# Kernel optimization log

Hardware: AMD Instinct MI355X
Metric: run time of the kernel (lower is better)

The kernel has to match this reference:

```python
import math
import jax, jax.numpy as jnp
import numpy as np

H, DK = 16, 64            # n_heads, d_kv
NUM_BUCKETS, MAX_DIST = 32, 128


def _relative_position_buckets(S):
    # Bidirectional (encoder) T5 bucketization of relative positions.
    ctx = jnp.arange(S, dtype=jnp.int32)[:, None]      # query positions
    mem = jnp.arange(S, dtype=jnp.int32)[None, :]      # key positions
    rp = mem - ctx                                     # [S, S]
    nb = NUM_BUCKETS // 2
    rb = (rp > 0).astype(jnp.int32) * nb
    n = jnp.abs(rp)
    max_exact = nb // 2
    is_small = n < max_exact
    large = max_exact + (
        jnp.log(jnp.maximum(n, 1).astype(jnp.float32) / max_exact)
        / math.log(MAX_DIST / max_exact)
        * (nb - max_exact)
    ).astype(jnp.int32)
    large = jnp.minimum(large, nb - 1)
    return rb + jnp.where(is_small, n, large)          # [S, S] int32


def setup_inputs() -> dict:
    key = jax.random.key(0)
    ks = jax.random.split(key, 6)
    B, S, D = 4, 1024, 1024
    inner = H * DK
    std = 0.02
    return {
        "hidden_states": jax.random.normal(ks[0], (B, S, D), jnp.float32),
        "Wq": jax.random.normal(ks[1], (inner, D), jnp.float32) * std,
        "Wk": jax.random.normal(ks[2], (inner, D), jnp.float32) * std,
        "Wv": jax.random.normal(ks[3], (inner, D), jnp.float32) * std,
        "Wo": jax.random.normal(ks[4], (D, inner), jnp.float32) * std,
        "rel_bias": jax.random.normal(ks[5], (NUM_BUCKETS, H), jnp.float32) * std,
    }


def reference(hidden_states, Wq, Wk, Wv, Wo, rel_bias):
    B, S, D = hidden_states.shape

    def proj(W):  # bias-free linear + split heads -> [B, H, S, DK]
        return (hidden_states @ W.T).reshape(B, S, H, DK).transpose(0, 2, 1, 3)

    q, k, v = proj(Wq), proj(Wk), proj(Wv)
    # T5: NO 1/sqrt(d) scaling
    scores = jnp.einsum("bhqd,bhkd->bhqk", q, k)       # [B, H, S, S]
    bias = rel_bias[_relative_position_buckets(S)]     # [S, S, H]
    scores = scores + bias.transpose(2, 0, 1)[None]    # broadcast over batch
    attn = jax.nn.softmax(scores, axis=-1)
    ctx = jnp.einsum("bhqk,bhkd->bhqd", attn, v)       # [B, H, S, DK]
    ctx = ctx.transpose(0, 2, 1, 3).reshape(B, S, H * DK)
    return ctx @ Wo.T                                  # [B, S, D]
```

## Files before the change

kernel.cpp:

```cpp
#include <hip/hip_runtime.h>

typedef _Float16 half8 __attribute__((ext_vector_type(8)));
typedef _Float16 half4_t __attribute__((ext_vector_type(4)));
typedef float f32x4 __attribute__((ext_vector_type(4)));

#define GK 1024
#define MEG (1024 * 1024)
#define LOG2E 1.44269504088896f

#define GLD16(gptr, lptr) \
    __builtin_amdgcn_global_load_lds((const __attribute__((address_space(1))) void*)(gptr), \
                                     (__attribute__((address_space(3))) void*)(lptr), 16, 0, 0)

__global__ void cvt_all_kernel(const float* __restrict__ hidden,
                               const float* __restrict__ Wq,
                               const float* __restrict__ Wk,
                               const float* __restrict__ Wv,
                               const float* __restrict__ Wo,
                               _Float16* __restrict__ ws) {
    int b = blockIdx.x;
    const float* src;
    _Float16* dst;
    if (b < 4096)      { src = hidden; dst = ws; }
    else if (b < 5120) { src = Wq; dst = ws + 4 * MEG; b -= 4096; }
    else if (b < 6144) { src = Wk; dst = ws + 5 * MEG; b -= 5120; }
    else if (b < 7168) { src = Wv; dst = ws + 6 * MEG; b -= 6144; }
    else               { src = Wo; dst = ws + 7 * MEG; b -= 7168; }
    int i = (b * 256 + threadIdx.x) * 4;
    f32x4 v = *(const f32x4*)(src + i);
    half4_t h;
    h[0] = (_Float16)v[0]; h[1] = (_Float16)v[1];
    h[2] = (_Float16)v[2]; h[3] = (_Float16)v[3];
    *(half4_t*)(dst + i) = h;
}

__global__ __launch_bounds__(256) void gemm_qkv_kernel(
    const _Float16* __restrict__ A,
    const _Float16* __restrict__ B0,
    const _Float16* __restrict__ B1,
    const _Float16* __restrict__ B2,
    _Float16* __restrict__ O0,
    _Float16* __restrict__ O1,
    _Float16* __restrict__ O2)
{
    int z = blockIdx.z;
    const _Float16* Bw = (z == 0) ? B0 : ((z == 1) ? B1 : B2);
    _Float16* Oh = (z == 0) ? O0 : ((z == 1) ? O1 : O2);

    __shared__ __attribute__((aligned(16))) _Float16 sA[2][128][32];
    __shared__ __attribute__((aligned(16))) _Float16 sB[2][128][32];

    const int tid = threadIdx.x;
    const int wave = tid >> 6, lane = tid & 63;
    const int quad = lane >> 4, l16 = lane & 15;
    const int wr = wave >> 1, wc = wave & 1;
    const int M0 = blockIdx.y * 128, N0 = blockIdx.x * 128;

    const int rl = lane >> 2;
    const int cl = (lane & 3) * 8;
    const size_t aRow0 = (size_t)(M0 + wave * 16 + rl) * GK + cl;
    const size_t aRow1 = aRow0 + (size_t)64 * GK;
    const size_t bRow0 = (size_t)(N0 + wave * 16 + rl) * GK + cl;
    const size_t bRow1 = bRow0 + (size_t)64 * GK;
    _Float16* ldsA[2][2] = {{&sA[0][wave * 16][0], &sA[0][64 + wave * 16][0]},
                            {&sA[1][wave * 16][0], &sA[1][64 + wave * 16][0]}};
    _Float16* ldsB[2][2] = {{&sB[0][wave * 16][0], &sB[0][64 + wave * 16][0]},
                            {&sB[1][wave * 16][0], &sB[1][64 + wave * 16][0]}};

    f32x4 acc[4][4] = {};

    for (int kt = 0; kt < GK / 64; ++kt) {
        const int ko = kt * 64;
        #pragma unroll
        for (int c = 0; c < 2; ++c) {
            GLD16(A + aRow0 + ko + c * 32, ldsA[c][0]);
            GLD16(A + aRow1 + ko + c * 32, ldsA[c][1]);
            GLD16(Bw + bRow0 + ko + c * 32, ldsB[c][0]);
            GLD16(Bw + bRow1 + ko + c * 32, ldsB[c][1]);
        }
        __syncthreads();
        #pragma unroll
        for (int c = 0; c < 2; ++c) {
            half8 af[4], bf[4];
            #pragma unroll
            for (int i = 0; i < 4; ++i)
                af[i] = *(const half8*)&sA[c][wr * 64 + i * 16 + l16][quad * 8];
            #pragma unroll
            for (int j = 0; j < 4; ++j)
                bf[j] = *(const half8*)&sB[c][wc * 64 + j * 16 + l16][quad * 8];
            #pragma unroll
            for (int i = 0; i < 4; ++i)
                #pragma unroll
                for (int j = 0; j < 4; ++j)
                    acc[i][j] = __builtin_amdgcn_mfma_f32_16x16x32_f16(af[i], bf[j], acc[i][j], 0, 0, 0);
        }
        __syncthreads();
    }

    #pragma unroll
    for (int i = 0; i < 4; ++i) {
        #pragma unroll
        for (int j = 0; j < 4; ++j) {
            #pragma unroll
            for (int r = 0; r < 4; ++r) {
                int m = M0 + wr * 64 + i * 16 + quad * 4 + r;
                int n = N0 + wc * 64 + j * 16 + l16;
                int b = m >> 10, s = m & 1023, hh = n >> 6, d = n & 63;
                Oh[((size_t)((b * 16 + hh) * 1024 + s)) * 64 + d] = (_Float16)acc[i][j][r];
            }
        }
    }
}

__global__ __launch_bounds__(256) void gemm_o_kernel(
    const _Float16* __restrict__ A,
    const _Float16* __restrict__ Bw,
    float* __restrict__ Of)
{
    __shared__ __attribute__((aligned(16))) _Float16 sA[2][64][32];
    __shared__ __attribute__((aligned(16))) _Float16 sB[2][128][32];

    const int tid = threadIdx.x;
    const int wave = tid >> 6, lane = tid & 63;
    const int quad = lane >> 4, l16 = lane & 15;
    const int M0 = blockIdx.y * 64, N0 = blockIdx.x * 128;

    const int rl = lane >> 2;
    const int cl = (lane & 3) * 8;
    const size_t aRow  = (size_t)(M0 + wave * 16 + rl) * GK + cl;
    const size_t bRow0 = (size_t)(N0 + wave * 16 + rl) * GK + cl;
    const size_t bRow1 = bRow0 + (size_t)64 * GK;
    _Float16* ldsA[2]    = {&sA[0][wave * 16][0], &sA[1][wave * 16][0]};
    _Float16* ldsB[2][2] = {{&sB[0][wave * 16][0], &sB[0][64 + wave * 16][0]},
                            {&sB[1][wave * 16][0], &sB[1][64 + wave * 16][0]}};

    f32x4 acc[4][2] = {};

    for (int kt = 0; kt < GK / 64; ++kt) {
        const int ko = kt * 64;
        #pragma unroll
        for (int c = 0; c < 2; ++c) {
            GLD16(A + aRow + ko + c * 32, ldsA[c]);
            GLD16(Bw + bRow0 + ko + c * 32, ldsB[c][0]);
            GLD16(Bw + bRow1 + ko + c * 32, ldsB[c][1]);
        }
        __syncthreads();
        #pragma unroll
        for (int c = 0; c < 2; ++c) {
            half8 af[4], bf[2];
            #pragma unroll
            for (int i = 0; i < 4; ++i)
                af[i] = *(const half8*)&sA[c][i * 16 + l16][quad * 8];
            #pragma unroll
            for (int j = 0; j < 2; ++j)
                bf[j] = *(const half8*)&sB[c][wave * 32 + j * 16 + l16][quad * 8];
            #pragma unroll
            for (int i = 0; i < 4; ++i)
                #pragma unroll
                for (int j = 0; j < 2; ++j)
                    acc[i][j] = __builtin_amdgcn_mfma_f32_16x16x32_f16(af[i], bf[j], acc[i][j], 0, 0, 0);
        }
        __syncthreads();
    }

    #pragma unroll
    for (int i = 0; i < 4; ++i) {
        #pragma unroll
        for (int j = 0; j < 2; ++j) {
            #pragma unroll
            for (int r = 0; r < 4; ++r) {
                int m = M0 + i * 16 + quad * 4 + r;
                int n = N0 + wave * 32 + j * 16 + l16;
                Of[(size_t)m * 1024 + n] = acc[i][j][r];
            }
        }
    }
}

__global__ __launch_bounds__(256) void transpose_v_kernel(
    const _Float16* __restrict__ V, _Float16* __restrict__ VT) {
    __shared__ __attribute__((aligned(16))) _Float16 sT[64][72];
    const int s0 = blockIdx.x * 64;
    const int bh = blockIdx.y;
    const _Float16* Vb = V + (size_t)bh * 1024 * 64 + (size_t)s0 * 64;
    _Float16* Tb = VT + (size_t)bh * 64 * 1024 + s0;
    const int r = threadIdx.x >> 3;
    const int c8 = (threadIdx.x & 7) * 8;
    #pragma unroll
    for (int p = 0; p < 2; ++p) {
        const int row = p * 32 + r;
        half8 v = *(const half8*)(Vb + (size_t)row * 64 + c8);
        #pragma unroll
        for (int e = 0; e < 8; ++e) sT[c8 + e][row] = v[e];
    }
    __syncthreads();
    #pragma unroll
    for (int p = 0; p < 2; ++p) {
        const int d = p * 32 + r;
        half8 o = *(const half8*)&sT[d][c8];
        *(half8*)(Tb + (size_t)d * 1024 + c8) = o;
    }
}

__global__ __launch_bounds__(256) void attn_kernel(
    const _Float16* __restrict__ Q,
    const _Float16* __restrict__ K,
    const _Float16* __restrict__ VT,
    const float* __restrict__ rel_bias,
    _Float16* __restrict__ ctx)
{
    const int S = 1024;
    const int qt = blockIdx.x;
    const int q0 = qt * 64;
    const int h = blockIdx.y;
    const int b = blockIdx.z;
    const int bh = b * 16 + h;
    const _Float16* Qh = Q + (size_t)bh * S * 64;
    const _Float16* Kh = K + (size_t)bh * S * 64;
    const _Float16* VTh = VT + (size_t)bh * 64 * S;

    __shared__ __attribute__((aligned(16))) _Float16 sQ[64][72];
    __shared__ __attribute__((aligned(16))) _Float16 sK[64][72];
    __shared__ __attribute__((aligned(16))) _Float16 sVt[64][72];
    __shared__ __attribute__((aligned(16))) _Float16 sP[4][16][72];
    __shared__ _Float16 sBias[1088];

    const int tid = threadIdx.x;
    const int wave = tid >> 6, lane = tid & 63;
    const int quad = lane >> 4, l16 = lane & 15;

    {
        int r = tid >> 3, c = (tid & 7) * 8;
        *(half8*)&sQ[r][c]      = *(const half8*)(Qh + (size_t)(q0 + r) * 64 + c);
        *(half8*)&sQ[r + 32][c] = *(const half8*)(Qh + (size_t)(q0 + r + 32) * 64 + c);
    }
    for (int i = tid; i < 1087; i += 256) {
        int delta = i - (q0 + 63);
        int rb = (delta > 0) ? 16 : 0;
        int n = (delta < 0) ? -delta : delta;
        int bucket;
        if (n < 8) bucket = rb + n;
        else bucket = rb + 8 + (n >= 12) + (n >= 16) + (n >= 23) + (n >= 32)
                             + (n >= 46) + (n >= 64) + (n >= 91);
        sBias[i] = (_Float16)rel_bias[bucket * 16 + h];
    }
    __syncthreads();

    half8 qf0 = *(const half8*)&sQ[wave * 16 + l16][quad * 8];
    half8 qf1 = *(const half8*)&sQ[wave * 16 + l16][32 + quad * 8];

    const int sr = tid >> 3;
    const int sc_ = (tid & 7) * 8;
    const _Float16* kp0 = Kh + (size_t)sr * 64 + sc_;
    const _Float16* kp1 = kp0 + (size_t)32 * 64;
    const _Float16* vp0 = VTh + (size_t)sr * S + sc_;
    const _Float16* vp1 = vp0 + (size_t)32 * S;
    _Float16* sKw0 = &sK[sr][sc_];
    _Float16* sKw1 = &sK[sr + 32][sc_];
    _Float16* sVw0 = &sVt[sr][sc_];
    _Float16* sVw1 = &sVt[sr + 32][sc_];

    half8 rk0 = *(const half8*)kp0;
    half8 rk1 = *(const half8*)kp1;
    half8 rv0 = *(const half8*)vp0;
    half8 rv1 = *(const half8*)vp1;
    kp0 += 4096; kp1 += 4096; vp0 += 64; vp1 += 64;

    float m_run = -INFINITY, l_run = 0.0f;
    f32x4 acc[4] = {};

    for (int kt = 0; kt < 16; ++kt) {
        __syncthreads();
        *(half8*)sKw0 = rk0;
        *(half8*)sKw1 = rk1;
        *(half8*)sVw0 = rv0;
        *(half8*)sVw1 = rv1;
        __syncthreads();
        if (kt < 15) {
            rk0 = *(const half8*)kp0;
            rk1 = *(const half8*)kp1;
            rv0 = *(const half8*)vp0;
            rv1 = *(const half8*)vp1;
            kp0 += 4096; kp1 += 4096; vp0 += 64; vp1 += 64;
        }

        f32x4 sc[4] = {};
        #pragma unroll
        for (int j = 0; j < 4; ++j) {
            half8 kf0 = *(const half8*)&sK[j * 16 + l16][quad * 8];
            half8 kf1 = *(const half8*)&sK[j * 16 + l16][32 + quad * 8];
            sc[j] = __builtin_amdgcn_mfma_f32_16x16x32_f16(kf0, qf0, sc[j], 0, 0, 0);
            sc[j] = __builtin_amdgcn_mfma_f32_16x16x32_f16(kf1, qf1, sc[j], 0, 0, 0);
        }

        const int bbase = kt * 64 + quad * 4 - wave * 16 - l16 + 63;
        float ps = 0.0f;
        if (kt <= qt - 3 || kt >= qt + 3) {
            const float cb = (float)sBias[bbase];
            float mx = fmaxf(fmaxf(fmaxf(sc[0][0], sc[0][1]), fmaxf(sc[0][2], sc[0][3])),
                             fmaxf(fmaxf(sc[1][0], sc[1][1]), fmaxf(sc[1][2], sc[1][3])));
            mx = fmaxf(mx, fmaxf(fmaxf(fmaxf(sc[2][0], sc[2][1]), fmaxf(sc[2][2], sc[2][3])),
                                 fmaxf(fmaxf(sc[3][0], sc[3][1]), fmaxf(sc[3][2], sc[3][3]))));
            mx = fmaxf(mx, __shfl_xor(mx, 16));
            mx = fmaxf(mx, __shfl_xor(mx, 32));
            float mnew = fmaxf(m_run, mx + cb);
            float alpha = __expf(m_run - mnew);
            m_run = mnew;
            const float kk = (cb - mnew) * LOG2E;
            #pragma unroll
            for (int j = 0; j < 4; ++j) {
                half4_t pw;
                #pragma unroll
                for (int r = 0; r < 4; ++r) {
                    float p = __builtin_exp2f(__builtin_fmaf(sc[j][r], LOG2E, kk));
                    ps += p;
                    pw[r] = (_Float16)p;
                }
                *(half4_t*)&sP[wave][l16][j * 16 + quad * 4] = pw;
            }
            l_run = l_run * alpha + ps;
            #pragma unroll
            for (int dt = 0; dt < 4; ++dt) acc[dt] *= alpha;
        } else {
            #pragma unroll
            for (int j = 0; j < 4; ++j)
                #pragma unroll
                for (int r = 0; r < 4; ++r)
                    sc[j][r] += (float)sBias[bbase + j * 16 + r];
            float mx = fmaxf(fmaxf(fmaxf(sc[0][0], sc[0][1]), fmaxf(sc[0][2], sc[0][3])),
                             fmaxf(fmaxf(sc[1][0], sc[1][1]), fmaxf(sc[1][2], sc[1][3])));
            mx = fmaxf(mx, fmaxf(fmaxf(fmaxf(sc[2][0], sc[2][1]), fmaxf(sc[2][2], sc[2][3])),
                                 fmaxf(fmaxf(sc[3][0], sc[3][1]), fmaxf(sc[3][2], sc[3][3]))));
            mx = fmaxf(mx, __shfl_xor(mx, 16));
            mx = fmaxf(mx, __shfl_xor(mx, 32));
            float mnew = fmaxf(m_run, mx);
            float alpha = __expf(m_run - mnew);
            m_run = mnew;
            #pragma unroll
            for (int j = 0; j < 4; ++j) {
                half4_t pw;
                #pragma unroll
                for (int r = 0; r < 4; ++r) {
                    float p = __expf(sc[j][r] - mnew);
                    ps += p;
                    pw[r] = (_Float16)p;
                }
                *(half4_t*)&sP[wave][l16][j * 16 + quad * 4] = pw;
            }
            l_run = l_run * alpha + ps;
            #pragma unroll
            for (int dt = 0; dt < 4; ++dt) acc[dt] *= alpha;
        }

        half8 pf0 = *(const half8*)&sP[wave][l16][quad * 8];
        half8 pf1 = *(const half8*)&sP[wave][l16][32 + quad * 8];
        #pragma unroll
        for (int dt = 0; dt < 4; ++dt) {
            half8 vf0 = *(const half8*)&sVt[dt * 16 + l16][quad * 8];
            half8 vf1 = *(const half8*)&sVt[dt * 16 + l16][32 + quad * 8];
            acc[dt] = __builtin_amdgcn_mfma_f32_16x16x32_f16(vf0, pf0, acc[dt], 0, 0, 0);
            acc[dt] = __builtin_amdgcn_mfma_f32_16x16x32_f16(vf1, pf1, acc[dt], 0, 0, 0);
        }
    }

    l_run += __shfl_xor(l_run, 16);
    l_run += __shfl_xor(l_run, 32);
    const float inv = 1.0f / l_run;
    const size_t qg = (size_t)(b * 1024 + q0 + wave * 16 + l16);
    #pragma unroll
    for (int dt = 0; dt < 4; ++dt) {
        half4_t o;
        #pragma unroll
        for (int r = 0; r < 4; ++r) o[r] = (_Float16)(acc[dt][r] * inv);
        *(half4_t*)&ctx[qg * 1024 + h * 64 + dt * 16 + quad * 4] = o;
    }
}

extern "C" void kernel_launch(void* const* d_in, const int* in_sizes, int n_in,
                              void* d_out, int out_size, void* d_ws, size_t ws_size,
                              hipStream_t stream) {
    const float* hidden   = (const float*)d_in[0];
    const float* Wq       = (const float*)d_in[1];
    const float* Wk       = (const float*)d_in[2];
    const float* Wv       = (const float*)d_in[3];
    const float* Wo       = (const float*)d_in[4];
    const float* rel_bias = (const float*)d_in[5];
    float* out = (float*)d_out;

    _Float16* ws    = (_Float16*)d_ws;
    _Float16* h16   = ws;
    _Float16* wq16  = ws + 4 * (size_t)MEG;
    _Float16* wk16  = ws + 5 * (size_t)MEG;
    _Float16* wv16  = ws + 6 * (size_t)MEG;
    _Float16* wo16  = ws + 7 * (size_t)MEG;
    _Float16* Qs    = ws + 8 * (size_t)MEG;
    _Float16* Ks    = ws + 12 * (size_t)MEG;
    _Float16* Vs    = ws + 16 * (size_t)MEG;
    _Float16* ctx16 = ws + 20 * (size_t)MEG;
    _Float16* VTs   = h16;

    cvt_all_kernel<<<8192, 256, 0, stream>>>(hidden, Wq, Wk, Wv, Wo, ws);

    gemm_qkv_kernel<<<dim3(8, 32, 3), 256, 0, stream>>>(
        h16, wq16, wk16, wv16, Qs, Ks, Vs);

    transpose_v_kernel<<<dim3(16, 64), 256, 0, stream>>>(Vs, VTs);

    attn_kernel<<<dim3(16, 16, 4), 256, 0, stream>>>(Qs, Ks, VTs, rel_bias, ctx16);

    gemm_o_kernel<<<dim3(8, 64), 256, 0, stream>>>(ctx16, wo16, out);
}
```

Measured before the change: 198.7 us.

## Process 128 queries per attention block, two 16-row groups per wave

Doubles the query tile of the attention kernel from 64 to 128 rows, so each wave handles two 16-query groups against the same K/V tile loaded once into shared memory. K and V fragments are read into registers once per key tile and reused for both groups, halving K/V global and LDS traffic per query. The grid shrinks to 512 blocks, and register and LDS use grow, which may lower occupancy and leave fewer blocks to fill the device.

```diff
diff --git a/kernel.cpp b/kernel.cpp
--- a/kernel.cpp
+++ b/kernel.cpp
@@ -211,7 +211,7 @@
 {
     const int S = 1024;
     const int qt = blockIdx.x;
-    const int q0 = qt * 64;
+    const int q0 = qt * 128;
     const int h = blockIdx.y;
     const int b = blockIdx.z;
     const int bh = b * 16 + h;
@@ -219,11 +219,11 @@
     const _Float16* Kh = K + (size_t)bh * S * 64;
     const _Float16* VTh = VT + (size_t)bh * 64 * S;
 
-    __shared__ __attribute__((aligned(16))) _Float16 sQ[64][72];
+    __shared__ __attribute__((aligned(16))) _Float16 sQ[128][72];
     __shared__ __attribute__((aligned(16))) _Float16 sK[64][72];
     __shared__ __attribute__((aligned(16))) _Float16 sVt[64][72];
-    __shared__ __attribute__((aligned(16))) _Float16 sP[4][16][72];
-    __shared__ _Float16 sBias[1088];
+    __shared__ __attribute__((aligned(16))) _Float16 sP[4][2][16][72];
+    __shared__ _Float16 sBias[1152];
 
     const int tid = threadIdx.x;
     const int wave = tid >> 6, lane = tid & 63;
@@ -231,11 +231,13 @@
 
     {
         int r = tid >> 3, c = (tid & 7) * 8;
-        *(half8*)&sQ[r][c]      = *(const half8*)(Qh + (size_t)(q0 + r) * 64 + c);
-        *(half8*)&sQ[r + 32][c] = *(const half8*)(Qh + (size_t)(q0 + r + 32) * 64 + c);
-    }
-    for (int i = tid; i < 1087; i += 256) {
-        int delta = i - (q0 + 63);
+        #pragma unroll
+        for (int p = 0; p < 4; ++p)
+            *(half8*)&sQ[r + p * 32][c] =
+                *(const half8*)(Qh + (size_t)(q0 + r + p * 32) * 64 + c);
+    }
+    for (int i = tid; i < 1151; i += 256) {
+        int delta = i - (q0 + 127);
         int rb = (delta > 0) ? 16 : 0;
         int n = (delta < 0) ? -delta : delta;
         int bucket;
@@ -246,8 +248,12 @@
     }
     __syncthreads();
 
-    half8 qf0 = *(const half8*)&sQ[wave * 16 + l16][quad * 8];
-    half8 qf1 = *(const half8*)&sQ[wave * 16 + l16][32 + quad * 8];
+    half8 qf[2][2];
+    #pragma unroll
+    for (int g = 0; g < 2; ++g) {
+        qf[g][0] = *(const half8*)&sQ[wave * 32 + g * 16 + l16][quad * 8];
+        qf[g][1] = *(const half8*)&sQ[wave * 32 + g * 16 + l16][32 + quad * 8];
+    }
 
     const int sr = tid >> 3;
     const int sc_ = (tid & 7) * 8;
@@ -266,8 +272,9 @@
     half8 rv1 = *(const half8*)vp1;
     kp0 += 4096; kp1 += 4096; vp0 += 64; vp1 += 64;
 
-    float m_run = -INFINITY, l_run = 0.0f;
-    f32x4 acc[4] = {};
+    float m_run[2] = {-INFINITY, -INFINITY};
+    float l_run[2] = {0.0f, 0.0f};
+    f32x4 acc[2][4] = {};
 
     for (int kt = 0; kt < 16; ++kt) {
         __syncthreads();
@@ -284,95 +291,112 @@
             kp0 += 4096; kp1 += 4096; vp0 += 64; vp1 += 64;
         }
 
-        f32x4 sc[4] = {};
+        half8 kf[8], vf[8];
         #pragma unroll
         for (int j = 0; j < 4; ++j) {
-            half8 kf0 = *(const half8*)&sK[j * 16 + l16][quad * 8];
-            half8 kf1 = *(const half8*)&sK[j * 16 + l16][32 + quad * 8];
-            sc[j] = __builtin_amdgcn_mfma_f32_16x16x32_f16(kf0, qf0, sc[j], 0, 0, 0);
-            sc[j] = __builtin_amdgcn_mfma_f32_16x16x32_f16(kf1, qf1, sc[j], 0, 0, 0);
-        }
-
-        const int bbase = kt * 64 + quad * 4 - wave * 16 - l16 + 63;
-        float ps = 0.0f;
-        if (kt <= qt - 3 || kt >= qt + 3) {
-            const float cb = (float)sBias[bbase];
-            float mx = fmaxf(fmaxf(fmaxf(sc[0][0], sc[0][1]), fmaxf(sc[0][2], sc[0][3])),
-                             fmaxf(fmaxf(sc[1][0], sc[1][1]), fmaxf(sc[1][2], sc[1][3])));
-            mx = fmaxf(mx, fmaxf(fmaxf(fmaxf(sc[2][0], sc[2][1]), fmaxf(sc[2][2], sc[2][3])),
-                                 fmaxf(fmaxf(sc[3][0], sc[3][1]), fmaxf(sc[3][2], sc[3][3]))));
-            mx = fmaxf(mx, __shfl_xor(mx, 16));
-            mx = fmaxf(mx, __shfl_xor(mx, 32));
-            float mnew = fmaxf(m_run, mx + cb);
-            float alpha = __expf(m_run - mnew);
-            m_run = mnew;
-            const float kk = (cb - mnew) * LOG2E;
+            kf[j * 2]     = *(const half8*)&sK[j * 16 + l16][quad * 8];
+            kf[j * 2 + 1] = *(const half8*)&sK[j * 16 + l16][32 + quad * 8];
+        }
+        #pragma unroll
+        for (int dt = 0; dt < 4; ++dt) {
+            vf[dt * 2]     = *(const half8*)&sVt[dt * 16 + l16][quad * 8];
+            vf[dt * 2 + 1] = *(const half8*)&sVt[dt * 16 + l16][32 + quad * 8];
+        }
+
+        const bool uni = (kt <= 2 * qt - 3) || (kt >= 2 * qt + 4);
+
+        #pragma unroll
+        for (int g = 0; g < 2; ++g) {
+            f32x4 sc[4] = {};
             #pragma unroll
             for (int j = 0; j < 4; ++j) {
-                half4_t pw;
-                #pragma unroll
-                for (int r = 0; r < 4; ++r) {
-                    float p = __builtin_exp2f(__builtin_fmaf(sc[j][r], LOG2E, kk));
-                    ps += p;
-                    pw[r] = (_Float16)p;
+                sc[j] = __builtin_amdgcn_mfma_f32_16x16x32_f16(kf[j * 2], qf[g][0], sc[j], 0, 0, 0);
+                sc[j] = __builtin_amdgcn_mfma_f32_16x16x32_f16(kf[j * 2 + 1], qf[g][1], sc[j], 0, 0, 0);
+            }
+
+            const int bbase = kt * 64 + quad * 4 - wave * 32 - g * 16 - l16 + 127;
+            float ps = 0.0f;
+            if (uni) {
+                const float cb = (float)sBias[bbase];
+                float mx = fmaxf(fmaxf(fmaxf(sc[0][0], sc[0][1]), fmaxf(sc[0][2], sc[0][3])),
+                                 fmaxf(fmaxf(sc[1][0], sc[1][1]), fmaxf(sc[1][2], sc[1][3])));
+                mx = fmaxf(mx, fmaxf(fmaxf(fmaxf(sc[2][0], sc[2][1]), fmaxf(sc[2][2], sc[2][3])),
+                                     fmaxf(fmaxf(sc[3][0], sc[3][1]), fmaxf(sc[3][2], sc[3][3]))));
+                mx = fmaxf(mx, __shfl_xor(mx, 16));
+                mx = fmaxf(mx, __shfl_xor(mx, 32));
+                float mnew = fmaxf(m_run[g], mx + cb);
+                float alpha = __expf(m_run[g] - mnew);
+                m_run[g] = mnew;
+                const float kk = (cb - mnew) * LOG2E;
+                #pragma unroll
+                for (int j = 0; j < 4; ++j) {
+                    half4_t pw;
+                    #pragma unroll
+                    for (int r = 0; r < 4; ++r) {
+                        float p = __builtin_exp2f(__builtin_fmaf(sc[j][r], LOG2E, kk));
+                        ps += p;
+                        pw[r] = (_Float16)p;
+                    }
+                    *(half4_t*)&sP[wave][g][l16][j * 16 + quad * 4] = pw;
                 }
-                *(half4_t*)&sP[wave][l16][j * 16 + quad * 4] = pw;
+                l_run[g] = l_run[g] * alpha + ps;
+                #pragma unroll
+                for (int dt = 0; dt < 4; ++dt) acc[g][dt] *= alpha;
+            } else {
+                #pragma unroll
+                for (int j = 0; j < 4; ++j)
+                    #pragma unroll
+                    for (int r = 0; r < 4; ++r)
+                        sc[j][r] += (float)sBias[bbase + j * 16 + r];
+                float mx = fmaxf(fmaxf(fmaxf(sc[0][0], sc[0][1]), fmaxf(sc[0][2], sc[0][3])),
+                                 fmaxf(fmaxf(sc[1][0], sc[1][1]), fmaxf(sc[1][2], sc[1][3])));
+                mx = fmaxf(mx, fmaxf(fmaxf(fmaxf(sc[2][0], sc[2][1]), fmaxf(sc[2][2], sc[2][3])),
+                                     fmaxf(fmaxf(sc[3][0], sc[3][1]), fmaxf(sc[3][2], sc[3][3]))));
+                mx = fmaxf(mx, __shfl_xor(mx, 16));
+                mx = fmaxf(mx, __shfl_xor(mx, 32));
+                float mnew = fmaxf(m_run[g], mx);
+                float alpha = __expf(m_run[g] - mnew);
+                m_run[g] = mnew;
+                #pragma unroll
+                for (int j = 0; j < 4; ++j) {
+                    half4_t pw;
+                    #pragma unroll
+                    for (int r = 0; r < 4; ++r) {
+                        float p = __expf(sc[j][r] - mnew);
+                        ps += p;
+                        pw[r] = (_Float16)p;
+                    }
+                    *(half4_t*)&sP[wave][g][l16][j * 16 + quad * 4] = pw;
+                }
+                l_run[g] = l_run[g] * alpha + ps;
+                #pragma unroll
+                for (int dt = 0; dt < 4; ++dt) acc[g][dt] *= alpha;
             }
-            l_run = l_run * alpha + ps;
-            #pragma unroll
-            for (int dt = 0; dt < 4; ++dt) acc[dt] *= alpha;
-        } else {
-            #pragma unroll
-            for (int j = 0; j < 4; ++j)
-                #pragma unroll
-                for (int r = 0; r < 4; ++r)
-                    sc[j][r] += (float)sBias[bbase + j * 16 + r];
-            float mx = fmaxf(fmaxf(fmaxf(sc[0][0], sc[0][1]), fmaxf(sc[0][2], sc[0][3])),
-                             fmaxf(fmaxf(sc[1][0], sc[1][1]), fmaxf(sc[1][2], sc[1][3])));
-            mx = fmaxf(mx, fmaxf(fmaxf(fmaxf(sc[2][0], sc[2][1]), fmaxf(sc[2][2], sc[2][3])),
-                                 fmaxf(fmaxf(sc[3][0], sc[3][1]), fmaxf(sc[3][2], sc[3][3]))));
-            mx = fmaxf(mx, __shfl_xor(mx, 16));
-            mx = fmaxf(mx, __shfl_xor(mx, 32));
-            float mnew = fmaxf(m_run, mx);
-            float alpha = __expf(m_run - mnew);
-            m_run = mnew;
-            #pragma unroll
-            for (int j = 0; j < 4; ++j) {
-                half4_t pw;
-                #pragma unroll
-                for (int r = 0; r < 4; ++r) {
-                    float p = __expf(sc[j][r] - mnew);
-                    ps += p;
-                    pw[r] = (_Float16)p;
-                }
-                *(half4_t*)&sP[wave][l16][j * 16 + quad * 4] = pw;
+
+            half8 pf0 = *(const half8*)&sP[wave][g][l16][quad * 8];
+            half8 pf1 = *(const half8*)&sP[wave][g][l16][32 + quad * 8];
+            #pragma unroll
+            for (int dt = 0; dt < 4; ++dt) {
+                acc[g][dt] = __builtin_amdgcn_mfma_f32_16x16x32_f16(vf[dt * 2], pf0, acc[g][dt], 0, 0, 0);
+                acc[g][dt] = __builtin_amdgcn_mfma_f32_16x16x32_f16(vf[dt * 2 + 1], pf1, acc[g][dt], 0, 0, 0);
             }
-            l_run = l_run * alpha + ps;
-            #pragma unroll
-            for (int dt = 0; dt < 4; ++dt) acc[dt] *= alpha;
-        }
-
-        half8 pf0 = *(const half8*)&sP[wave][l16][quad * 8];
-        half8 pf1 = *(const half8*)&sP[wave][l16][32 + quad * 8];
+        }
+    }
+
+    #pragma unroll
+    for (int g = 0; g < 2; ++g) {
+        float l = l_run[g];
+        l += __shfl_xor(l, 16);
+        l += __shfl_xor(l, 32);
+        const float inv = 1.0f / l;
+        const size_t qg = (size_t)(b * 1024 + q0 + wave * 32 + g * 16 + l16);
         #pragma unroll
         for (int dt = 0; dt < 4; ++dt) {
-            half8 vf0 = *(const half8*)&sVt[dt * 16 + l16][quad * 8];
-            half8 vf1 = *(const half8*)&sVt[dt * 16 + l16][32 + quad * 8];
-            acc[dt] = __builtin_amdgcn_mfma_f32_16x16x32_f16(vf0, pf0, acc[dt], 0, 0, 0);
-            acc[dt] = __builtin_amdgcn_mfma_f32_16x16x32_f16(vf1, pf1, acc[dt], 0, 0, 0);
-        }
-    }
-
-    l_run += __shfl_xor(l_run, 16);
-    l_run += __shfl_xor(l_run, 32);
-    const float inv = 1.0f / l_run;
-    const size_t qg = (size_t)(b * 1024 + q0 + wave * 16 + l16);
-    #pragma unroll
-    for (int dt = 0; dt < 4; ++dt) {
-        half4_t o;
-        #pragma unroll
-        for (int r = 0; r < 4; ++r) o[r] = (_Float16)(acc[dt][r] * inv);
-        *(half4_t*)&ctx[qg * 1024 + h * 64 + dt * 16 + quad * 4] = o;
+            half4_t o;
+            #pragma unroll
+            for (int r = 0; r < 4; ++r) o[r] = (_Float16)(acc[g][dt][r] * inv);
+            *(half4_t*)&ctx[qg * 1024 + h * 64 + dt * 16 + quad * 4] = o;
+        }
     }
 }
 
@@ -406,7 +430,7 @@
 
     transpose_v_kernel<<<dim3(16, 64), 256, 0, stream>>>(Vs, VTs);
 
-    attn_kernel<<<dim3(16, 16, 4), 256, 0, stream>>>(Qs, Ks, VTs, rel_bias, ctx16);
+    attn_kernel<<<dim3(8, 16, 4), 256, 0, stream>>>(Qs, Ks, VTs, rel_bias, ctx16);
 
     gemm_o_kernel<<<dim3(8, 64), 256, 0, stream>>>(ctx16, wo16, out);
 }
```

Result: slower. 205.0 us (+3.2%).
